# Performance work log

Hardware: AMD Instinct MI355X
Metric: run time of the kernel (lower is better)

## Reference

```python
import jax, jax.numpy as jnp
import numpy as np

WINDOW = 8
HEADS = 12
HEAD_DIM = 64
DISP = WINDOW // 2  # cyclic shift displacement
WS2 = WINDOW * WINDOW


def _rel_indices():
    idx = np.array([[x, y] for x in range(WINDOW) for y in range(WINDOW)])  # (ws2,2)
    rel = idx[None, :, :] - idx[:, None, :] + (WINDOW - 1)  # (ws2,ws2,2)
    return rel


def _create_mask(upper_lower, left_right):
    m = np.zeros((WS2, WS2), dtype=np.float32)
    d = DISP
    if upper_lower:
        m[-d * WINDOW:, :-d * WINDOW] = -np.inf
        m[:-d * WINDOW, -d * WINDOW:] = -np.inf
    if left_right:
        m4 = m.reshape(WINDOW, WINDOW, WINDOW, WINDOW)
        m4[:, -d:, :, :-d] = -np.inf
        m4[:, :-d, :, -d:] = -np.inf
        m = m4.reshape(WS2, WS2)
    return m


def _window_masks(n_h, n_w):
    # per-window additive mask, (n_h*n_w, ws2, ws2)
    ul = _create_mask(True, False)
    lr = _create_mask(False, True)
    masks = np.zeros((n_h * n_w, WS2, WS2), dtype=np.float32)
    masks[-n_w:] += ul                 # last row of windows
    masks[n_w - 1::n_w] += lr          # last column of windows
    return masks


def _to_windows(x, n_h, n_w):
    # x: (b, c, h, w) -> (b, heads, n_windows, ws2, head_dim)
    b = x.shape[0]
    x = x.reshape(b, HEADS, HEAD_DIM, n_h, WINDOW, n_w, WINDOW)
    x = x.transpose(0, 1, 3, 5, 4, 6, 2)
    return x.reshape(b, HEADS, n_h * n_w, WS2, HEAD_DIM)


def setup_inputs() -> dict:
    key = jax.random.key(0)
    ks = jax.random.split(key, 8)
    B, H, W, C = 8, 64, 64, HEADS * HEAD_DIM
    return {
        "q_feat": jax.random.normal(ks[0], (B, H * W, C), dtype=jnp.float32),
        "k_feat": jax.random.normal(ks[1], (B, H * W, C), dtype=jnp.float32),
        "v_feat": jax.random.normal(ks[2], (B, H * W, C), dtype=jnp.float32),
        "Wq": jax.random.normal(ks[3], (HEAD_DIM, HEAD_DIM), dtype=jnp.float32) * 0.05,
        "Wk": jax.random.normal(ks[4], (HEAD_DIM, HEAD_DIM), dtype=jnp.float32) * 0.05,
        "Wv": jax.random.normal(ks[5], (HEAD_DIM, HEAD_DIM), dtype=jnp.float32) * 0.05,
        "Wlin": jax.random.normal(ks[6], (HEAD_DIM, HEAD_DIM), dtype=jnp.float32) * 0.05,
        "pe": jax.random.normal(ks[7], (2 * WINDOW - 1, 2 * WINDOW - 1), dtype=jnp.float32),
        "h": 64,
        "w": 64,
    }


def reference(q_feat, k_feat, v_feat, Wq, Wk, Wv, Wlin, pe, h, w):
    b, hw, c = q_feat.shape
    n_h, n_w = h // WINDOW, w // WINDOW
    rel = _rel_indices()
    win_mask = jnp.asarray(_window_masks(n_h, n_w))  # (nwin, ws2, ws2)

    def to_img(f):  # (b, h*w, c) -> (b, c, h, w)
        return f.transpose(0, 2, 1).reshape(b, c, h, w)

    qi = jnp.roll(to_img(q_feat), (-DISP, -DISP), axis=(2, 3))
    ki = jnp.roll(to_img(k_feat), (-DISP, -DISP), axis=(2, 3))
    vi = jnp.roll(to_img(v_feat), (-DISP, -DISP), axis=(2, 3))

    qw = _to_windows(qi, n_h, n_w)  # (b, heads, nwin, ws2, hd)
    kw = _to_windows(ki, n_h, n_w)
    vw = _to_windows(vi, n_h, n_w)

    q = jnp.einsum('bhnsd,ed->bhnse', qw, Wq)
    k = jnp.einsum('bhnsd,ed->bhnse', kw, Wk)
    v = jnp.einsum('bhnsd,ed->bhnse', vw, Wv)

    qk = jnp.einsum('bhnqd,bhnkd->bhnqk', q, k) / np.sqrt(HEAD_DIM).astype(np.float32)
    bias = pe[rel[:, :, 0], rel[:, :, 1]]  # (ws2, ws2)
    qk = qk + bias[None, None, None] + win_mask[None, None]

    attn = jax.nn.softmax(qk, axis=-1)
    out = jnp.einsum('bhnqk,bhnkd->bhnqd', attn, v)
    out = jnp.einsum('bhnsd,ed->bhnse', out, Wlin)

    # windows back to image: (b,heads,nwin,ws2,hd) -> (b,c,h,w)
    out = out.transpose(0, 1, 4, 2, 3).reshape(b, c, n_h, n_w, WINDOW, WINDOW)
    out = out.transpose(0, 1, 2, 4, 3, 5).reshape(b, c, h, w)
    out = jnp.roll(out, (DISP, DISP), axis=(2, 3))
    out = out.reshape(b, c, h * w).transpose(0, 2, 1)  # (b, h*w, c)
    return out, attn
```

## Files before the change

kernel.cpp:

```cpp
#include <hip/hip_runtime.h>
#include <hip/hip_bf16.h>

typedef __bf16 bf16x8 __attribute__((ext_vector_type(8)));
typedef float f32x4 __attribute__((ext_vector_type(4)));
typedef float f32x8 __attribute__((ext_vector_type(8)));

#define MFMA16(a, b, c) __builtin_amdgcn_mfma_f32_16x16x32_bf16((a), (b), (c), 0, 0, 0)

static __device__ __forceinline__ unsigned short f2b(float f) {
    union { float f; unsigned int u; } v; v.f = f;
    unsigned int r = v.u + 0x7FFFu + ((v.u >> 16) & 1u);
    return (unsigned short)(r >> 16);
}

static __device__ __forceinline__ bf16x8 cvt8(const float* p) {
    f32x8 v = *reinterpret_cast<const f32x8*>(p);
    bf16x8 r;
    #pragma unroll
    for (int i = 0; i < 8; ++i) r[i] = (__bf16)v[i];
    return r;
}

__global__ __launch_bounds__(256) void precompute_mn(
    const float* __restrict__ Wq, const float* __restrict__ Wk,
    const float* __restrict__ Wv, const float* __restrict__ Wl,
    unsigned short* __restrict__ ws)
{
    __shared__ float A[4096], B[4096];
    const int bid = blockIdx.x;
    const int which = bid >> 2;
    const int rq = bid & 3;
    const int tid = threadIdx.x;
    for (int i = tid; i < 4096; i += 256) {
        A[i] = which ? Wl[i] : Wq[i];
        B[i] = which ? Wv[i] : Wk[i];
    }
    __syncthreads();
    const int row = rq * 16 + (tid >> 4);
    const int c0  = tid & 15;
    float acc[4] = {0, 0, 0, 0};
    if (which == 0) {
        for (int e = 0; e < 64; ++e) {
            const float s = B[e * 64 + row];
            #pragma unroll
            for (int i = 0; i < 4; ++i) acc[i] += A[e * 64 + c0 + 16 * i] * s;
        }
    } else {
        for (int c = 0; c < 64; ++c) {
            const float s = A[row * 64 + c];
            #pragma unroll
            for (int i = 0; i < 4; ++i) acc[i] += s * B[c * 64 + c0 + 16 * i];
        }
    }
    #pragma unroll
    for (int i = 0; i < 4; ++i)
        ws[which * 4096 + row * 64 + c0 + 16 * i] = f2b(acc[i]);
}

#define PITCH 68

__global__ __launch_bounds__(512) void swca_fused(
    const float* __restrict__ qf,
    const float* __restrict__ kf,
    const float* __restrict__ vf,
    const unsigned short* __restrict__ Mt,
    const unsigned short* __restrict__ Nw,
    const float* __restrict__ pe,
    float* __restrict__ out,
    float* __restrict__ attn,
    int nblk2)
{
    __shared__ unsigned short kwS[2][64][PITCH];
    __shared__ unsigned short vwT[2][64][PITCH];
    __shared__ unsigned short As[2][64][PITCH];

    int bid = blockIdx.x;
    const int nper = nblk2 >> 3;
    const int task2 = (bid & 7) * nper + (bid >> 3);

    const int tid = threadIdx.x;
    const int h2  = tid >> 8;
    int task = task2 * 2 + h2;

    const int head = task % 12; task /= 12;
    const int win  = task & 63;
    const int b    = task >> 6;
    const int wy = win >> 3, wx = win & 7;

    const int tt   = tid & 255;
    const int wid  = tt >> 6;
    const int lane = tt & 63;
    const int lg   = lane >> 4;
    const int lc   = lane & 15;
    const int srow = wid * 16 + lc;

    const int sy = srow >> 3, sx = srow & 7;
    const int gy = (wy * 8 + sy + 4) & 63;
    const int gx = (wx * 8 + sx + 4) & 63;
    const long rowbase = ((long)b * 4096 + gy * 64 + gx) * 768 + head * 64;

    auto ld8 = [](const unsigned short* p) -> bf16x8 {
        return *reinterpret_cast<const bf16x8*>(p);
    };

    bf16x8 qa0 = cvt8(qf + rowbase + lg * 8);
    bf16x8 qa1 = cvt8(qf + rowbase + 32 + lg * 8);
    bf16x8 kb0 = cvt8(kf + rowbase + lg * 8);
    bf16x8 kb1 = cvt8(kf + rowbase + 32 + lg * 8);
    f32x8 vb0 = *reinterpret_cast<const f32x8*>(vf + rowbase + lg * 8);
    f32x8 vb1 = *reinterpret_cast<const f32x8*>(vf + rowbase + 32 + lg * 8);

    *reinterpret_cast<bf16x8*>(&kwS[h2][srow][lg * 8]) = kb0;
    *reinterpret_cast<bf16x8*>(&kwS[h2][srow][32 + lg * 8]) = kb1;
    #pragma unroll
    for (int i = 0; i < 8; ++i) {
        vwT[h2][lg * 8 + i][srow] = f2b(vb0[i]);
        vwT[h2][32 + lg * 8 + i][srow] = f2b(vb1[i]);
    }
    __syncthreads();

    {
        f32x4 acc[4] = {};
        #pragma unroll
        for (int t = 0; t < 4; ++t) {
            acc[t] = MFMA16(qa0, ld8(Mt + (t * 16 + lc) * 64 + lg * 8), acc[t]);
            acc[t] = MFMA16(qa1, ld8(Mt + (t * 16 + lc) * 64 + 32 + lg * 8), acc[t]);
        }
        #pragma unroll
        for (int t = 0; t < 4; ++t)
            #pragma unroll
            for (int j = 0; j < 4; ++j)
                As[h2][wid * 16 + lg * 4 + j][t * 16 + lc] = f2b(acc[t][j]);
    }

    f32x4 accS[4] = {};
    {
        bf16x8 a0 = ld8(&As[h2][srow][lg * 8]);
        bf16x8 a1 = ld8(&As[h2][srow][32 + lg * 8]);
        #pragma unroll
        for (int t = 0; t < 4; ++t) {
            accS[t] = MFMA16(a0, ld8(&kwS[h2][t * 16 + lc][lg * 8]), accS[t]);
            accS[t] = MFMA16(a1, ld8(&kwS[h2][t * 16 + lc][32 + lg * 8]), accS[t]);
        }
    }
    const int r0 = wid * 16 + lg * 4;
    {
        float sv[4][4];
        #pragma unroll
        for (int t = 0; t < 4; ++t) {
            const int c = t * 16 + lc, ky = c >> 3, kx = c & 7;
            #pragma unroll
            for (int j = 0; j < 4; ++j) {
                const int r = r0 + j, qy = r >> 3, qx = r & 7;
                const float biasv = pe[(ky - qy + 7) * 15 + (kx - qx + 7)];
                const bool msk = ((wy == 7) && (((qy ^ ky) & 4) != 0)) ||
                                 ((wx == 7) && (((qx ^ kx) & 4) != 0));
                sv[t][j] = msk ? -__builtin_inff() : accS[t][j] * 0.125f + biasv;
            }
        }
        float pv[4][4];
        #pragma unroll
        for (int j = 0; j < 4; ++j) {
            float mx = fmaxf(fmaxf(sv[0][j], sv[1][j]), fmaxf(sv[2][j], sv[3][j]));
            mx = fmaxf(mx, __shfl_xor(mx, 1));
            mx = fmaxf(mx, __shfl_xor(mx, 2));
            mx = fmaxf(mx, __shfl_xor(mx, 4));
            mx = fmaxf(mx, __shfl_xor(mx, 8));
            const float e0 = __expf(sv[0][j] - mx);
            const float e1 = __expf(sv[1][j] - mx);
            const float e2 = __expf(sv[2][j] - mx);
            const float e3 = __expf(sv[3][j] - mx);
            float sm = (e0 + e1) + (e2 + e3);
            sm += __shfl_xor(sm, 1);
            sm += __shfl_xor(sm, 2);
            sm += __shfl_xor(sm, 4);
            sm += __shfl_xor(sm, 8);
            const float inv = 1.0f / sm;
            pv[0][j] = e0 * inv; pv[1][j] = e1 * inv;
            pv[2][j] = e2 * inv; pv[3][j] = e3 * inv;
        }
        const long abase0 = ((((long)b * 12 + head) * 64 + win) * 64 + r0) * 64;
        #pragma unroll
        for (int j = 0; j < 4; ++j)
            #pragma unroll
            for (int t = 0; t < 4; ++t)
                attn[abase0 + (long)j * 64 + t * 16 + lc] = pv[t][j];
        #pragma unroll
        for (int t = 0; t < 4; ++t)
            #pragma unroll
            for (int j = 0; j < 4; ++j)
                As[h2][r0 + j][t * 16 + lc] = f2b(pv[t][j]);
    }

    {
        bf16x8 a0 = ld8(&As[h2][srow][lg * 8]);
        bf16x8 a1 = ld8(&As[h2][srow][32 + lg * 8]);
        f32x4 acc[4] = {};
        #pragma unroll
        for (int t = 0; t < 4; ++t) {
            acc[t] = MFMA16(a0, ld8(&vwT[h2][t * 16 + lc][lg * 8]), acc[t]);
            acc[t] = MFMA16(a1, ld8(&vwT[h2][t * 16 + lc][32 + lg * 8]), acc[t]);
        }
        #pragma unroll
        for (int t = 0; t < 4; ++t)
            #pragma unroll
            for (int j = 0; j < 4; ++j)
                As[h2][wid * 16 + lg * 4 + j][t * 16 + lc] = f2b(acc[t][j]);
    }

    {
        bf16x8 a0 = ld8(&As[h2][srow][lg * 8]);
        bf16x8 a1 = ld8(&As[h2][srow][32 + lg * 8]);
        f32x4 acc[4] = {};
        #pragma unroll
        for (int t = 0; t < 4; ++t) {
            acc[t] = MFMA16(a0, ld8(Nw + (t * 16 + lc) * 64 + lg * 8), acc[t]);
            acc[t] = MFMA16(a1, ld8(Nw + (t * 16 + lc) * 64 + 32 + lg * 8), acc[t]);
        }
        #pragma unroll
        for (int j = 0; j < 4; ++j) {
            const int r = r0 + j, ry = r >> 3, rx = r & 7;
            const int oy = (wy * 8 + ry + 4) & 63;
            const int ox = (wx * 8 + rx + 4) & 63;
            const long obase = ((long)b * 4096 + oy * 64 + ox) * 768 + head * 64;
            #pragma unroll
            for (int t = 0; t < 4; ++t)
                out[obase + t * 16 + lc] = acc[t][j];
        }
    }
}

extern "C" void kernel_launch(void* const* d_in, const int* in_sizes, int n_in,
                              void* d_out, int out_size, void* d_ws, size_t ws_size,
                              hipStream_t stream) {
    const float* qf = (const float*)d_in[0];
    const float* kf = (const float*)d_in[1];
    const float* vf = (const float*)d_in[2];
    const float* Wq = (const float*)d_in[3];
    const float* Wk = (const float*)d_in[4];
    const float* Wv = (const float*)d_in[5];
    const float* Wl = (const float*)d_in[6];
    const float* pe = (const float*)d_in[7];

    const int B = in_sizes[0] / (4096 * 768);
    float* outp = (float*)d_out;
    float* attnp = outp + (size_t)B * 4096 * 768;
    unsigned short* ws = (unsigned short*)d_ws;

    precompute_mn<<<8, 256, 0, stream>>>(Wq, Wk, Wv, Wl, ws);

    const int nblk2 = B * 768 / 2;
    swca_fused<<<nblk2, 512, 0, stream>>>(qf, kf, vf, ws, ws + 4096, pe,
                                          outp, attnp, nblk2);
}
```

Measured before the change: 139.1 us.

## Make blocks persistent over several tasks with register prefetch of next inputs

Each 256-thread block now processes six consecutive (batch,window,head) tasks in a loop. It prefetches the next task's q/k/v rows into registers while computing the current one, which is meant to hide global load latency. The attention matrix is now written back from the bf16 shared tile as vectorized float4 stores instead of scattered scalar stores, so stored attn values are bf16-rounded. The change also drops the blockIdx swizzle across XCDs and adds two barriers per task.

```diff
diff --git a/kernel.cpp b/kernel.cpp
--- a/kernel.cpp
+++ b/kernel.cpp
@@ -4,6 +4,7 @@
 typedef __bf16 bf16x8 __attribute__((ext_vector_type(8)));
 typedef float f32x4 __attribute__((ext_vector_type(4)));
 typedef float f32x8 __attribute__((ext_vector_type(8)));
+typedef unsigned short u16x8 __attribute__((ext_vector_type(8)));
 
 #define MFMA16(a, b, c) __builtin_amdgcn_mfma_f32_16x16x32_bf16((a), (b), (c), 0, 0, 0)
 
@@ -12,9 +13,11 @@
     unsigned int r = v.u + 0x7FFFu + ((v.u >> 16) & 1u);
     return (unsigned short)(r >> 16);
 }
-
-static __device__ __forceinline__ bf16x8 cvt8(const float* p) {
-    f32x8 v = *reinterpret_cast<const f32x8*>(p);
+static __device__ __forceinline__ float b2f(unsigned short s) {
+    union { unsigned int u; float f; } v; v.u = ((unsigned int)s) << 16;
+    return v.f;
+}
+static __device__ __forceinline__ bf16x8 cvtv(f32x8 v) {
     bf16x8 r;
     #pragma unroll
     for (int i = 0; i < 8; ++i) r[i] = (__bf16)v[i];
@@ -58,8 +61,9 @@
 }
 
 #define PITCH 68
-
-__global__ __launch_bounds__(512) void swca_fused(
+#define NTASK 6
+
+__global__ __launch_bounds__(256, 4) void swca_fused(
     const float* __restrict__ qf,
     const float* __restrict__ kf,
     const float* __restrict__ vf,
@@ -67,166 +71,210 @@
     const unsigned short* __restrict__ Nw,
     const float* __restrict__ pe,
     float* __restrict__ out,
-    float* __restrict__ attn,
-    int nblk2)
+    float* __restrict__ attn)
 {
-    __shared__ unsigned short kwS[2][64][PITCH];
-    __shared__ unsigned short vwT[2][64][PITCH];
-    __shared__ unsigned short As[2][64][PITCH];
-
-    int bid = blockIdx.x;
-    const int nper = nblk2 >> 3;
-    const int task2 = (bid & 7) * nper + (bid >> 3);
-
-    const int tid = threadIdx.x;
-    const int h2  = tid >> 8;
-    int task = task2 * 2 + h2;
-
-    const int head = task % 12; task /= 12;
-    const int win  = task & 63;
-    const int b    = task >> 6;
-    const int wy = win >> 3, wx = win & 7;
-
-    const int tt   = tid & 255;
-    const int wid  = tt >> 6;
-    const int lane = tt & 63;
+    __shared__ unsigned short kwS[64][PITCH];
+    __shared__ unsigned short vwT[64][PITCH];
+    __shared__ unsigned short As[64][PITCH];
+
+    const int tid  = threadIdx.x;
+    const int wid  = tid >> 6;
+    const int lane = tid & 63;
     const int lg   = lane >> 4;
     const int lc   = lane & 15;
     const int srow = wid * 16 + lc;
-
     const int sy = srow >> 3, sx = srow & 7;
-    const int gy = (wy * 8 + sy + 4) & 63;
-    const int gx = (wx * 8 + sx + 4) & 63;
-    const long rowbase = ((long)b * 4096 + gy * 64 + gx) * 768 + head * 64;
+    const int r0 = wid * 16 + lg * 4;
 
     auto ld8 = [](const unsigned short* p) -> bf16x8 {
         return *reinterpret_cast<const bf16x8*>(p);
     };
 
-    bf16x8 qa0 = cvt8(qf + rowbase + lg * 8);
-    bf16x8 qa1 = cvt8(qf + rowbase + 32 + lg * 8);
-    bf16x8 kb0 = cvt8(kf + rowbase + lg * 8);
-    bf16x8 kb1 = cvt8(kf + rowbase + 32 + lg * 8);
-    f32x8 vb0 = *reinterpret_cast<const f32x8*>(vf + rowbase + lg * 8);
-    f32x8 vb1 = *reinterpret_cast<const f32x8*>(vf + rowbase + 32 + lg * 8);
-
-    *reinterpret_cast<bf16x8*>(&kwS[h2][srow][lg * 8]) = kb0;
-    *reinterpret_cast<bf16x8*>(&kwS[h2][srow][32 + lg * 8]) = kb1;
+    int task = blockIdx.x * NTASK;
+
+    int headC = task % 12; { }
+    int t2 = task / 12;
+    int winC = t2 & 63, bC = t2 >> 6;
+    long rbC;
+    {
+        const int wy = winC >> 3, wx = winC & 7;
+        const int gy = (wy * 8 + sy + 4) & 63;
+        const int gx = (wx * 8 + sx + 4) & 63;
+        rbC = ((long)bC * 4096 + gy * 64 + gx) * 768 + headC * 64;
+    }
+    f32x8 cq0 = *reinterpret_cast<const f32x8*>(qf + rbC + lg * 8);
+    f32x8 cq1 = *reinterpret_cast<const f32x8*>(qf + rbC + 32 + lg * 8);
+    f32x8 ck0 = *reinterpret_cast<const f32x8*>(kf + rbC + lg * 8);
+    f32x8 ck1 = *reinterpret_cast<const f32x8*>(kf + rbC + 32 + lg * 8);
+    f32x8 cv0 = *reinterpret_cast<const f32x8*>(vf + rbC + lg * 8);
+    f32x8 cv1 = *reinterpret_cast<const f32x8*>(vf + rbC + 32 + lg * 8);
+
+    *reinterpret_cast<bf16x8*>(&kwS[srow][lg * 8]) = cvtv(ck0);
+    *reinterpret_cast<bf16x8*>(&kwS[srow][32 + lg * 8]) = cvtv(ck1);
     #pragma unroll
     for (int i = 0; i < 8; ++i) {
-        vwT[h2][lg * 8 + i][srow] = f2b(vb0[i]);
-        vwT[h2][32 + lg * 8 + i][srow] = f2b(vb1[i]);
+        vwT[lg * 8 + i][srow] = f2b(cv0[i]);
+        vwT[32 + lg * 8 + i][srow] = f2b(cv1[i]);
     }
     __syncthreads();
 
-    {
-        f32x4 acc[4] = {};
-        #pragma unroll
-        for (int t = 0; t < 4; ++t) {
-            acc[t] = MFMA16(qa0, ld8(Mt + (t * 16 + lc) * 64 + lg * 8), acc[t]);
-            acc[t] = MFMA16(qa1, ld8(Mt + (t * 16 + lc) * 64 + 32 + lg * 8), acc[t]);
-        }
-        #pragma unroll
-        for (int t = 0; t < 4; ++t)
-            #pragma unroll
-            for (int j = 0; j < 4; ++j)
-                As[h2][wid * 16 + lg * 4 + j][t * 16 + lc] = f2b(acc[t][j]);
-    }
-
-    f32x4 accS[4] = {};
-    {
-        bf16x8 a0 = ld8(&As[h2][srow][lg * 8]);
-        bf16x8 a1 = ld8(&As[h2][srow][32 + lg * 8]);
-        #pragma unroll
-        for (int t = 0; t < 4; ++t) {
-            accS[t] = MFMA16(a0, ld8(&kwS[h2][t * 16 + lc][lg * 8]), accS[t]);
-            accS[t] = MFMA16(a1, ld8(&kwS[h2][t * 16 + lc][32 + lg * 8]), accS[t]);
-        }
-    }
-    const int r0 = wid * 16 + lg * 4;
-    {
-        float sv[4][4];
-        #pragma unroll
-        for (int t = 0; t < 4; ++t) {
-            const int c = t * 16 + lc, ky = c >> 3, kx = c & 7;
+    for (int it = 0; it < NTASK; ++it) {
+        f32x8 nq0 = {}, nq1 = {}, nk0 = {}, nk1 = {}, nv0 = {}, nv1 = {};
+        int headN = 0, winN = 0, bN = 0;
+        long rbN = 0;
+        if (it + 1 < NTASK) {
+            const int taskN = task + 1;
+            headN = taskN % 12;
+            const int t2n = taskN / 12;
+            winN = t2n & 63; bN = t2n >> 6;
+            const int wy = winN >> 3, wx = winN & 7;
+            const int gy = (wy * 8 + sy + 4) & 63;
+            const int gx = (wx * 8 + sx + 4) & 63;
+            rbN = ((long)bN * 4096 + gy * 64 + gx) * 768 + headN * 64;
+            nq0 = *reinterpret_cast<const f32x8*>(qf + rbN + lg * 8);
+            nq1 = *reinterpret_cast<const f32x8*>(qf + rbN + 32 + lg * 8);
+            nk0 = *reinterpret_cast<const f32x8*>(kf + rbN + lg * 8);
+            nk1 = *reinterpret_cast<const f32x8*>(kf + rbN + 32 + lg * 8);
+            nv0 = *reinterpret_cast<const f32x8*>(vf + rbN + lg * 8);
+            nv1 = *reinterpret_cast<const f32x8*>(vf + rbN + 32 + lg * 8);
+        }
+        const int wy = winC >> 3, wx = winC & 7;
+
+        {
+            bf16x8 qa0 = cvtv(cq0), qa1 = cvtv(cq1);
+            f32x4 acc[4] = {};
+            #pragma unroll
+            for (int t = 0; t < 4; ++t) {
+                acc[t] = MFMA16(qa0, ld8(Mt + (t * 16 + lc) * 64 + lg * 8), acc[t]);
+                acc[t] = MFMA16(qa1, ld8(Mt + (t * 16 + lc) * 64 + 32 + lg * 8), acc[t]);
+            }
+            #pragma unroll
+            for (int t = 0; t < 4; ++t)
+                #pragma unroll
+                for (int j = 0; j < 4; ++j)
+                    As[wid * 16 + lg * 4 + j][t * 16 + lc] = f2b(acc[t][j]);
+        }
+
+        f32x4 accS[4] = {};
+        {
+            bf16x8 a0 = ld8(&As[srow][lg * 8]);
+            bf16x8 a1 = ld8(&As[srow][32 + lg * 8]);
+            #pragma unroll
+            for (int t = 0; t < 4; ++t) {
+                accS[t] = MFMA16(a0, ld8(&kwS[t * 16 + lc][lg * 8]), accS[t]);
+                accS[t] = MFMA16(a1, ld8(&kwS[t * 16 + lc][32 + lg * 8]), accS[t]);
+            }
+        }
+        {
+            float sv[4][4];
+            #pragma unroll
+            for (int t = 0; t < 4; ++t) {
+                const int c = t * 16 + lc, ky = c >> 3, kx = c & 7;
+                #pragma unroll
+                for (int j = 0; j < 4; ++j) {
+                    const int r = r0 + j, qy = r >> 3, qx = r & 7;
+                    const float biasv = pe[(ky - qy + 7) * 15 + (kx - qx + 7)];
+                    const bool msk = ((wy == 7) && (((qy ^ ky) & 4) != 0)) ||
+                                     ((wx == 7) && (((qx ^ kx) & 4) != 0));
+                    sv[t][j] = msk ? -__builtin_inff() : accS[t][j] * 0.125f + biasv;
+                }
+            }
             #pragma unroll
             for (int j = 0; j < 4; ++j) {
-                const int r = r0 + j, qy = r >> 3, qx = r & 7;
-                const float biasv = pe[(ky - qy + 7) * 15 + (kx - qx + 7)];
-                const bool msk = ((wy == 7) && (((qy ^ ky) & 4) != 0)) ||
-                                 ((wx == 7) && (((qx ^ kx) & 4) != 0));
-                sv[t][j] = msk ? -__builtin_inff() : accS[t][j] * 0.125f + biasv;
-            }
-        }
-        float pv[4][4];
-        #pragma unroll
-        for (int j = 0; j < 4; ++j) {
-            float mx = fmaxf(fmaxf(sv[0][j], sv[1][j]), fmaxf(sv[2][j], sv[3][j]));
-            mx = fmaxf(mx, __shfl_xor(mx, 1));
-            mx = fmaxf(mx, __shfl_xor(mx, 2));
-            mx = fmaxf(mx, __shfl_xor(mx, 4));
-            mx = fmaxf(mx, __shfl_xor(mx, 8));
-            const float e0 = __expf(sv[0][j] - mx);
-            const float e1 = __expf(sv[1][j] - mx);
-            const float e2 = __expf(sv[2][j] - mx);
-            const float e3 = __expf(sv[3][j] - mx);
-            float sm = (e0 + e1) + (e2 + e3);
-            sm += __shfl_xor(sm, 1);
-            sm += __shfl_xor(sm, 2);
-            sm += __shfl_xor(sm, 4);
-            sm += __shfl_xor(sm, 8);
-            const float inv = 1.0f / sm;
-            pv[0][j] = e0 * inv; pv[1][j] = e1 * inv;
-            pv[2][j] = e2 * inv; pv[3][j] = e3 * inv;
-        }
-        const long abase0 = ((((long)b * 12 + head) * 64 + win) * 64 + r0) * 64;
-        #pragma unroll
-        for (int j = 0; j < 4; ++j)
+                float mx = fmaxf(fmaxf(sv[0][j], sv[1][j]), fmaxf(sv[2][j], sv[3][j]));
+                mx = fmaxf(mx, __shfl_xor(mx, 1));
+                mx = fmaxf(mx, __shfl_xor(mx, 2));
+                mx = fmaxf(mx, __shfl_xor(mx, 4));
+                mx = fmaxf(mx, __shfl_xor(mx, 8));
+                const float e0 = __expf(sv[0][j] - mx);
+                const float e1 = __expf(sv[1][j] - mx);
+                const float e2 = __expf(sv[2][j] - mx);
+                const float e3 = __expf(sv[3][j] - mx);
+                float sm = (e0 + e1) + (e2 + e3);
+                sm += __shfl_xor(sm, 1);
+                sm += __shfl_xor(sm, 2);
+                sm += __shfl_xor(sm, 4);
+                sm += __shfl_xor(sm, 8);
+                const float inv = 1.0f / sm;
+                As[r0 + j][0 * 16 + lc] = f2b(e0 * inv);
+                As[r0 + j][1 * 16 + lc] = f2b(e1 * inv);
+                As[r0 + j][2 * 16 + lc] = f2b(e2 * inv);
+                As[r0 + j][3 * 16 + lc] = f2b(e3 * inv);
+            }
+        }
+
+        {
+            bf16x8 a0 = ld8(&As[srow][lg * 8]);
+            bf16x8 a1 = ld8(&As[srow][32 + lg * 8]);
+
+            {
+                const int lr = wid * 16 + (lane >> 2);
+                const int c0 = (lane & 3) * 16;
+                u16x8 p0 = *reinterpret_cast<const u16x8*>(&As[lr][c0]);
+                u16x8 p1 = *reinterpret_cast<const u16x8*>(&As[lr][c0 + 8]);
+                const long abase = ((((long)bC * 12 + headC) * 64 + winC) * 64 + lr) * 64 + c0;
+                f32x4 o0, o1, o2, o3;
+                #pragma unroll
+                for (int i = 0; i < 4; ++i) { o0[i] = b2f(p0[i]); o1[i] = b2f(p0[4 + i]); }
+                #pragma unroll
+                for (int i = 0; i < 4; ++i) { o2[i] = b2f(p1[i]); o3[i] = b2f(p1[4 + i]); }
+                *reinterpret_cast<f32x4*>(attn + abase)      = o0;
+                *reinterpret_cast<f32x4*>(attn + abase + 4)  = o1;
+                *reinterpret_cast<f32x4*>(attn + abase + 8)  = o2;
+                *reinterpret_cast<f32x4*>(attn + abase + 12) = o3;
+            }
+
+            f32x4 acc[4] = {};
+            #pragma unroll
+            for (int t = 0; t < 4; ++t) {
+                acc[t] = MFMA16(a0, ld8(&vwT[t * 16 + lc][lg * 8]), acc[t]);
+                acc[t] = MFMA16(a1, ld8(&vwT[t * 16 + lc][32 + lg * 8]), acc[t]);
+            }
             #pragma unroll
             for (int t = 0; t < 4; ++t)
-                attn[abase0 + (long)j * 64 + t * 16 + lc] = pv[t][j];
-        #pragma unroll
-        for (int t = 0; t < 4; ++t)
-            #pragma unroll
-            for (int j = 0; j < 4; ++j)
-                As[h2][r0 + j][t * 16 + lc] = f2b(pv[t][j]);
-    }
-
-    {
-        bf16x8 a0 = ld8(&As[h2][srow][lg * 8]);
-        bf16x8 a1 = ld8(&As[h2][srow][32 + lg * 8]);
-        f32x4 acc[4] = {};
-        #pragma unroll
-        for (int t = 0; t < 4; ++t) {
-            acc[t] = MFMA16(a0, ld8(&vwT[h2][t * 16 + lc][lg * 8]), acc[t]);
-            acc[t] = MFMA16(a1, ld8(&vwT[h2][t * 16 + lc][32 + lg * 8]), acc[t]);
-        }
-        #pragma unroll
-        for (int t = 0; t < 4; ++t)
-            #pragma unroll
-            for (int j = 0; j < 4; ++j)
-                As[h2][wid * 16 + lg * 4 + j][t * 16 + lc] = f2b(acc[t][j]);
-    }
-
-    {
-        bf16x8 a0 = ld8(&As[h2][srow][lg * 8]);
-        bf16x8 a1 = ld8(&As[h2][srow][32 + lg * 8]);
-        f32x4 acc[4] = {};
-        #pragma unroll
-        for (int t = 0; t < 4; ++t) {
-            acc[t] = MFMA16(a0, ld8(Nw + (t * 16 + lc) * 64 + lg * 8), acc[t]);
-            acc[t] = MFMA16(a1, ld8(Nw + (t * 16 + lc) * 64 + 32 + lg * 8), acc[t]);
-        }
-        #pragma unroll
-        for (int j = 0; j < 4; ++j) {
-            const int r = r0 + j, ry = r >> 3, rx = r & 7;
-            const int oy = (wy * 8 + ry + 4) & 63;
-            const int ox = (wx * 8 + rx + 4) & 63;
-            const long obase = ((long)b * 4096 + oy * 64 + ox) * 768 + head * 64;
-            #pragma unroll
-            for (int t = 0; t < 4; ++t)
-                out[obase + t * 16 + lc] = acc[t][j];
-        }
+                #pragma unroll
+                for (int j = 0; j < 4; ++j)
+                    As[wid * 16 + lg * 4 + j][t * 16 + lc] = f2b(acc[t][j]);
+        }
+
+        __syncthreads();
+
+        if (it + 1 < NTASK) {
+            *reinterpret_cast<bf16x8*>(&kwS[srow][lg * 8]) = cvtv(nk0);
+            *reinterpret_cast<bf16x8*>(&kwS[srow][32 + lg * 8]) = cvtv(nk1);
+            #pragma unroll
+            for (int i = 0; i < 8; ++i) {
+                vwT[lg * 8 + i][srow] = f2b(nv0[i]);
+                vwT[32 + lg * 8 + i][srow] = f2b(nv1[i]);
+            }
+        }
+
+        {
+            bf16x8 a0 = ld8(&As[srow][lg * 8]);
+            bf16x8 a1 = ld8(&As[srow][32 + lg * 8]);
+            f32x4 acc[4] = {};
+            #pragma unroll
+            for (int t = 0; t < 4; ++t) {
+                acc[t] = MFMA16(a0, ld8(Nw + (t * 16 + lc) * 64 + lg * 8), acc[t]);
+                acc[t] = MFMA16(a1, ld8(Nw + (t * 16 + lc) * 64 + 32 + lg * 8), acc[t]);
+            }
+            #pragma unroll
+            for (int j = 0; j < 4; ++j) {
+                const int r = r0 + j, ry = r >> 3, rx = r & 7;
+                const int oy = (wy * 8 + ry + 4) & 63;
+                const int ox = (wx * 8 + rx + 4) & 63;
+                const long obase = ((long)bC * 4096 + oy * 64 + ox) * 768 + headC * 64;
+                #pragma unroll
+                for (int t = 0; t < 4; ++t)
+                    out[obase + t * 16 + lc] = acc[t][j];
+            }
+        }
+
+        __syncthreads();
+
+        cq0 = nq0; cq1 = nq1;
+        headC = headN; winC = winN; bC = bN;
+        task = task + 1;
     }
 }
 
@@ -249,7 +297,7 @@
 
     precompute_mn<<<8, 256, 0, stream>>>(Wq, Wk, Wv, Wl, ws);
 
-    const int nblk2 = B * 768 / 2;
-    swca_fused<<<nblk2, 512, 0, stream>>>(qf, kf, vf, ws, ws + 4096, pe,
-                                          outp, attnp, nblk2);
-}
+    const int nblk = B * 768 / NTASK;
+    swca_fused<<<nblk, 256, 0, stream>>>(qf, kf, vf, ws, ws + 4096, pe,
+                                         outp, attnp);
+}
```

New measurement: 183.6 us. 32.0% more time.

## Apply combined weight matrices to K and V instead of Q and output

Applied to the files above, without the earlier changes.

Reassociates the fused projections so the combined Wq/Wk matrix multiplies K and the combined Wv/Wlin matrix multiplies V before attention. Q then feeds the score MFMA directly from registers, and the separate output-projection MFMA stage after P·V goes away, along with one LDS round trip. The attention-probability store is also restaged through LDS so each lane writes contiguous 16-float vectors instead of scattered scalars. The precompute kernel is changed to produce the transposed combined matrix that the new ordering needs, and rounding points shift slightly because of the new bf16 staging.

```diff
diff --git a/kernel.cpp b/kernel.cpp
--- a/kernel.cpp
+++ b/kernel.cpp
@@ -4,6 +4,7 @@
 typedef __bf16 bf16x8 __attribute__((ext_vector_type(8)));
 typedef float f32x4 __attribute__((ext_vector_type(4)));
 typedef float f32x8 __attribute__((ext_vector_type(8)));
+typedef unsigned short u16x8 __attribute__((ext_vector_type(8)));
 
 #define MFMA16(a, b, c) __builtin_amdgcn_mfma_f32_16x16x32_bf16((a), (b), (c), 0, 0, 0)
 
@@ -12,9 +13,11 @@
     unsigned int r = v.u + 0x7FFFu + ((v.u >> 16) & 1u);
     return (unsigned short)(r >> 16);
 }
-
-static __device__ __forceinline__ bf16x8 cvt8(const float* p) {
-    f32x8 v = *reinterpret_cast<const f32x8*>(p);
+static __device__ __forceinline__ float b2f(unsigned short s) {
+    union { unsigned int u; float f; } v; v.u = ((unsigned int)s) << 16;
+    return v.f;
+}
+static __device__ __forceinline__ bf16x8 cvtv(f32x8 v) {
     bf16x8 r;
     #pragma unroll
     for (int i = 0; i < 8; ++i) r[i] = (__bf16)v[i];
@@ -41,9 +44,9 @@
     float acc[4] = {0, 0, 0, 0};
     if (which == 0) {
         for (int e = 0; e < 64; ++e) {
-            const float s = B[e * 64 + row];
-            #pragma unroll
-            for (int i = 0; i < 4; ++i) acc[i] += A[e * 64 + c0 + 16 * i] * s;
+            const float s = A[e * 64 + row];
+            #pragma unroll
+            for (int i = 0; i < 4; ++i) acc[i] += s * B[e * 64 + c0 + 16 * i];
         }
     } else {
         for (int c = 0; c < 64; ++c) {
@@ -63,15 +66,15 @@
     const float* __restrict__ qf,
     const float* __restrict__ kf,
     const float* __restrict__ vf,
-    const unsigned short* __restrict__ Mt,
+    const unsigned short* __restrict__ Mw,
     const unsigned short* __restrict__ Nw,
     const float* __restrict__ pe,
     float* __restrict__ out,
     float* __restrict__ attn,
     int nblk2)
 {
-    __shared__ unsigned short kwS[2][64][PITCH];
-    __shared__ unsigned short vwT[2][64][PITCH];
+    __shared__ unsigned short kmS[2][64][PITCH];
+    __shared__ unsigned short vnT[2][64][PITCH];
     __shared__ unsigned short As[2][64][PITCH];
 
     int bid = blockIdx.x;
@@ -103,44 +106,47 @@
         return *reinterpret_cast<const bf16x8*>(p);
     };
 
-    bf16x8 qa0 = cvt8(qf + rowbase + lg * 8);
-    bf16x8 qa1 = cvt8(qf + rowbase + 32 + lg * 8);
-    bf16x8 kb0 = cvt8(kf + rowbase + lg * 8);
-    bf16x8 kb1 = cvt8(kf + rowbase + 32 + lg * 8);
-    f32x8 vb0 = *reinterpret_cast<const f32x8*>(vf + rowbase + lg * 8);
-    f32x8 vb1 = *reinterpret_cast<const f32x8*>(vf + rowbase + 32 + lg * 8);
-
-    *reinterpret_cast<bf16x8*>(&kwS[h2][srow][lg * 8]) = kb0;
-    *reinterpret_cast<bf16x8*>(&kwS[h2][srow][32 + lg * 8]) = kb1;
-    #pragma unroll
-    for (int i = 0; i < 8; ++i) {
-        vwT[h2][lg * 8 + i][srow] = f2b(vb0[i]);
-        vwT[h2][32 + lg * 8 + i][srow] = f2b(vb1[i]);
+    bf16x8 kb0 = cvtv(*reinterpret_cast<const f32x8*>(kf + rowbase + lg * 8));
+    bf16x8 kb1 = cvtv(*reinterpret_cast<const f32x8*>(kf + rowbase + 32 + lg * 8));
+    bf16x8 vb0 = cvtv(*reinterpret_cast<const f32x8*>(vf + rowbase + lg * 8));
+    bf16x8 vb1 = cvtv(*reinterpret_cast<const f32x8*>(vf + rowbase + 32 + lg * 8));
+    bf16x8 qa0 = cvtv(*reinterpret_cast<const f32x8*>(qf + rowbase + lg * 8));
+    bf16x8 qa1 = cvtv(*reinterpret_cast<const f32x8*>(qf + rowbase + 32 + lg * 8));
+
+    {
+        f32x4 acc[4] = {};
+        #pragma unroll
+        for (int t = 0; t < 4; ++t) {
+            acc[t] = MFMA16(kb0, ld8(Mw + (t * 16 + lc) * 64 + lg * 8), acc[t]);
+            acc[t] = MFMA16(kb1, ld8(Mw + (t * 16 + lc) * 64 + 32 + lg * 8), acc[t]);
+        }
+        #pragma unroll
+        for (int t = 0; t < 4; ++t)
+            #pragma unroll
+            for (int j = 0; j < 4; ++j)
+                kmS[h2][wid * 16 + lg * 4 + j][t * 16 + lc] = f2b(acc[t][j]);
+    }
+    {
+        f32x4 acc[4] = {};
+        #pragma unroll
+        for (int t = 0; t < 4; ++t) {
+            acc[t] = MFMA16(vb0, ld8(Nw + (t * 16 + lc) * 64 + lg * 8), acc[t]);
+            acc[t] = MFMA16(vb1, ld8(Nw + (t * 16 + lc) * 64 + 32 + lg * 8), acc[t]);
+        }
+        #pragma unroll
+        for (int t = 0; t < 4; ++t)
+            #pragma unroll
+            for (int j = 0; j < 4; ++j)
+                vnT[h2][t * 16 + lc][wid * 16 + lg * 4 + j] = f2b(acc[t][j]);
     }
     __syncthreads();
 
-    {
-        f32x4 acc[4] = {};
-        #pragma unroll
-        for (int t = 0; t < 4; ++t) {
-            acc[t] = MFMA16(qa0, ld8(Mt + (t * 16 + lc) * 64 + lg * 8), acc[t]);
-            acc[t] = MFMA16(qa1, ld8(Mt + (t * 16 + lc) * 64 + 32 + lg * 8), acc[t]);
-        }
-        #pragma unroll
-        for (int t = 0; t < 4; ++t)
-            #pragma unroll
-            for (int j = 0; j < 4; ++j)
-                As[h2][wid * 16 + lg * 4 + j][t * 16 + lc] = f2b(acc[t][j]);
-    }
-
     f32x4 accS[4] = {};
     {
-        bf16x8 a0 = ld8(&As[h2][srow][lg * 8]);
-        bf16x8 a1 = ld8(&As[h2][srow][32 + lg * 8]);
-        #pragma unroll
-        for (int t = 0; t < 4; ++t) {
-            accS[t] = MFMA16(a0, ld8(&kwS[h2][t * 16 + lc][lg * 8]), accS[t]);
-            accS[t] = MFMA16(a1, ld8(&kwS[h2][t * 16 + lc][32 + lg * 8]), accS[t]);
+        #pragma unroll
+        for (int t = 0; t < 4; ++t) {
+            accS[t] = MFMA16(qa0, ld8(&kmS[h2][t * 16 + lc][lg * 8]), accS[t]);
+            accS[t] = MFMA16(qa1, ld8(&kmS[h2][t * 16 + lc][32 + lg * 8]), accS[t]);
         }
     }
     const int r0 = wid * 16 + lg * 4;
@@ -158,7 +164,6 @@
                 sv[t][j] = msk ? -__builtin_inff() : accS[t][j] * 0.125f + biasv;
             }
         }
-        float pv[4][4];
         #pragma unroll
         for (int j = 0; j < 4; ++j) {
             float mx = fmaxf(fmaxf(sv[0][j], sv[1][j]), fmaxf(sv[2][j], sv[3][j]));
@@ -176,20 +181,28 @@
             sm += __shfl_xor(sm, 4);
             sm += __shfl_xor(sm, 8);
             const float inv = 1.0f / sm;
-            pv[0][j] = e0 * inv; pv[1][j] = e1 * inv;
-            pv[2][j] = e2 * inv; pv[3][j] = e3 * inv;
-        }
-        const long abase0 = ((((long)b * 12 + head) * 64 + win) * 64 + r0) * 64;
-        #pragma unroll
-        for (int j = 0; j < 4; ++j)
-            #pragma unroll
-            for (int t = 0; t < 4; ++t)
-                attn[abase0 + (long)j * 64 + t * 16 + lc] = pv[t][j];
-        #pragma unroll
-        for (int t = 0; t < 4; ++t)
-            #pragma unroll
-            for (int j = 0; j < 4; ++j)
-                As[h2][r0 + j][t * 16 + lc] = f2b(pv[t][j]);
+            As[h2][r0 + j][0 * 16 + lc] = f2b(e0 * inv);
+            As[h2][r0 + j][1 * 16 + lc] = f2b(e1 * inv);
+            As[h2][r0 + j][2 * 16 + lc] = f2b(e2 * inv);
+            As[h2][r0 + j][3 * 16 + lc] = f2b(e3 * inv);
+        }
+    }
+
+    {
+        const int lr = wid * 16 + (lane >> 2);
+        const int c0 = (lane & 3) * 16;
+        u16x8 p0 = *reinterpret_cast<const u16x8*>(&As[h2][lr][c0]);
+        u16x8 p1 = *reinterpret_cast<const u16x8*>(&As[h2][lr][c0 + 8]);
+        const long abase = ((((long)b * 12 + head) * 64 + win) * 64 + lr) * 64 + c0;
+        f32x4 o0, o1, o2, o3;
+        #pragma unroll
+        for (int i = 0; i < 4; ++i) { o0[i] = b2f(p0[i]); o1[i] = b2f(p0[4 + i]); }
+        #pragma unroll
+        for (int i = 0; i < 4; ++i) { o2[i] = b2f(p1[i]); o3[i] = b2f(p1[4 + i]); }
+        *reinterpret_cast<f32x4*>(attn + abase)      = o0;
+        *reinterpret_cast<f32x4*>(attn + abase + 4)  = o1;
+        *reinterpret_cast<f32x4*>(attn + abase + 8)  = o2;
+        *reinterpret_cast<f32x4*>(attn + abase + 12) = o3;
     }
 
     {
@@ -198,24 +211,8 @@
         f32x4 acc[4] = {};
         #pragma unroll
         for (int t = 0; t < 4; ++t) {
-            acc[t] = MFMA16(a0, ld8(&vwT[h2][t * 16 + lc][lg * 8]), acc[t]);
-            acc[t] = MFMA16(a1, ld8(&vwT[h2][t * 16 + lc][32 + lg * 8]), acc[t]);
-        }
-        #pragma unroll
-        for (int t = 0; t < 4; ++t)
-            #pragma unroll
-            for (int j = 0; j < 4; ++j)
-                As[h2][wid * 16 + lg * 4 + j][t * 16 + lc] = f2b(acc[t][j]);
-    }
-
-    {
-        bf16x8 a0 = ld8(&As[h2][srow][lg * 8]);
-        bf16x8 a1 = ld8(&As[h2][srow][32 + lg * 8]);
-        f32x4 acc[4] = {};
-        #pragma unroll
-        for (int t = 0; t < 4; ++t) {
-            acc[t] = MFMA16(a0, ld8(Nw + (t * 16 + lc) * 64 + lg * 8), acc[t]);
-            acc[t] = MFMA16(a1, ld8(Nw + (t * 16 + lc) * 64 + 32 + lg * 8), acc[t]);
+            acc[t] = MFMA16(a0, ld8(&vnT[h2][t * 16 + lc][lg * 8]), acc[t]);
+            acc[t] = MFMA16(a1, ld8(&vnT[h2][t * 16 + lc][32 + lg * 8]), acc[t]);
         }
         #pragma unroll
         for (int j = 0; j < 4; ++j) {
```

After: 143.0 us, median of 3. 2.9% more time.
